# Optimization experiments

Hardware: AMD Instinct MI355X
Metric: run time of the kernel (lower is better)

Reference implementation:

```python
import jax, jax.numpy as jnp
import numpy as np

ALPHA = 0.2  # LeakyReLU negative slope used throughout
NEG = -9e15


def _leaky(x, a=ALPHA):
    return jnp.where(x >= 0, x, a * x)


def _gat_layer(h, adj, W, a, concat):
    # h: [N, Fin], W: [Fin, Fout], a: [2*Fout, 1]
    Wh = h @ W                                   # [N, Fout]
    d = W.shape[-1]
    e = _leaky(Wh @ a[:d] + (Wh @ a[d:]).T)      # [N, N]
    att = jax.nn.softmax(jnp.where(adj > 0, e, NEG), axis=1)
    out = att @ Wh                               # [N, Fout]
    return jax.nn.elu(out) if concat else out


def setup_inputs() -> dict:
    key = jax.random.key(0)
    ks = jax.random.split(key, 24)
    N, F, H, D1, O1 = 4096, 512, 4, 256, 64
    x = jax.random.normal(ks[0], (N, F), dtype=jnp.float32)
    adj = jax.random.bernoulli(ks[1], 0.02, (N, N))
    adj = (adj | adj.T | jnp.eye(N, dtype=bool)).astype(jnp.float32)
    observation = jax.random.randint(ks[2], (1, N), 0, 2, dtype=jnp.int32)
    s_mat = jax.random.uniform(ks[3], (N, N), dtype=jnp.float32)
    theta = jax.random.uniform(ks[4], (1, F), dtype=jnp.float32)
    g = lambda k, s, sc: (jax.random.normal(k, s, dtype=jnp.float32) * sc)
    return {
        'x': x, 'adj': adj, 'observation': observation, 's_mat': s_mat,
        'theta': theta,
        'Wh0': g(ks[5], (H, F, D1), 0.05), 'ah0': g(ks[6], (H, 2 * D1, 1), 0.05),
        'Wh1': g(ks[7], (H, D1, D1), 0.05), 'ah1': g(ks[8], (H, 2 * D1, 1), 0.05),
        'Wo0': g(ks[9], (H * D1, O1), 0.05), 'ao0': g(ks[10], (2 * O1, 1), 0.05),
        'Wo1': g(ks[11], (O1, 1), 0.2), 'ao1': g(ks[12], (2, 1), 0.2),
        'dW': g(ks[13], (2, 10), 0.5), 'dW0': g(ks[14], (1, 10), 0.5),
        'dW1': g(ks[15], (10, 20), 0.5), 'dW01': g(ks[16], (1, 20), 0.5),
        'dW2': g(ks[17], (20, 10), 0.5), 'dW02': g(ks[18], (1, 10), 0.5),
        'dV': g(ks[19], (10, 1), 0.5), 'dV0': g(ks[20], (1, 1), 0.5),
    }


def reference(x, adj, observation, s_mat, theta, Wh0, ah0, Wh1, ah1,
              Wo0, ao0, Wo1, ao1, dW, dW0, dW1, dW01, dW2, dW02, dV, dV0):
    # mergeState: add theta to rows in the seed set (observation[0] == 1)
    seed = (observation[0] == 1).astype(x.dtype)[:, None]  # [N,1]
    h_in = x + seed * theta

    # multi-head 2-layer attention stacks (concat=True -> elu inside)
    def head(W0, a0, W1, a1):
        h = _gat_layer(h_in, adj, W0, a0, True)
        return _gat_layer(h, adj, W1, a1, True)

    hh = jax.vmap(head)(Wh0, ah0, Wh1, ah1)                 # [H, N, D1]
    hcat = jnp.transpose(hh, (1, 0, 2)).reshape(h_in.shape[0], -1)  # [N, H*D1]

    # output attention stack (concat=False), then elu (GAT.forward)
    h = _gat_layer(hcat, adj, Wo0, ao0, False)
    h = _gat_layer(h, adj, Wo1, ao1, False)
    h_ = jax.nn.elu(h)                                      # [N, 1]

    # GAT_degree v2: degreeNN over [h_, degree]
    d_v = s_mat.sum(axis=1, keepdims=True)                  # [N, 1]
    x_ = jnp.concatenate([h_, d_v], axis=1)                 # [N, 2]
    h0 = _leaky(x_ @ dW + dW0)
    h1 = _leaky(h0 @ dW1 + dW01)
    h2 = _leaky(h1 @ dW2 + dW02)
    return _leaky(h2 @ dV + dV0)                            # [N, 1]
```

## Files before the change

### kernel.cpp

```cpp
#include <hip/hip_runtime.h>
#include <hip/hip_bf16.h>
#include <math.h>

#define MAXDEG 512

typedef short v8s __attribute__((ext_vector_type(8)));
typedef float v4f __attribute__((ext_vector_type(4)));
typedef float v2f __attribute__((ext_vector_type(2)));

__device__ __forceinline__ float blockReduceSum(float v) {
    __shared__ float sh[8];
    int lane = threadIdx.x & 63, w = threadIdx.x >> 6;
    for (int o = 32; o > 0; o >>= 1) v += __shfl_down(v, o);
    __syncthreads();
    if (lane == 0) sh[w] = v;
    __syncthreads();
    if (w == 0) {
        int nw = (blockDim.x + 63) >> 6;
        v = (lane < nw) ? sh[lane] : 0.f;
        for (int o = 4; o > 0; o >>= 1) v += __shfl_down(v, o);
        if (lane == 0) sh[0] = v;
    }
    __syncthreads();
    return sh[0];
}

__device__ __forceinline__ float blockReduceMax(float v) {
    __shared__ float sh[8];
    int lane = threadIdx.x & 63, w = threadIdx.x >> 6;
    for (int o = 32; o > 0; o >>= 1) v = fmaxf(v, __shfl_down(v, o));
    __syncthreads();
    if (lane == 0) sh[w] = v;
    __syncthreads();
    if (w == 0) {
        int nw = (blockDim.x + 63) >> 6;
        v = (lane < nw) ? sh[lane] : -3.4e38f;
        for (int o = 4; o > 0; o >>= 1) v = fmaxf(v, __shfl_down(v, o));
        if (lane == 0) sh[0] = v;
    }
    __syncthreads();
    return sh[0];
}

__device__ __forceinline__ v2f bf2f(unsigned int u) {
    union { unsigned int u; float f; } lo, hi;
    lo.u = u << 16;
    hi.u = u & 0xffff0000u;
    return (v2f){lo.f, hi.f};
}

__device__ __forceinline__ void acc_add(v2f* a, float p, const uint4& r) {
    v2f pp = (v2f){p, p};
    a[0] += pp * bf2f(r.x);
    a[1] += pp * bf2f(r.y);
    a[2] += pp * bf2f(r.z);
    a[3] += pp * bf2f(r.w);
}


__global__ void zero_f32(float* __restrict__ p, int n) {
    int i = blockIdx.x * 256 + threadIdx.x;
    if (i < n) p[i] = 0.f;
}

__global__ void csr_rowsum(const float* __restrict__ adj, const float* __restrict__ s,
                           int* __restrict__ colIdx, int* __restrict__ deg,
                           float* __restrict__ dv, int N) {
    int row = blockIdx.x;
    __shared__ int cnt;
    if (threadIdx.x == 0) cnt = 0;
    __syncthreads();
    const float* ar = adj + (size_t)row * N;
    const float* sr = s + (size_t)row * N;
    int* outp = colIdx + (size_t)row * MAXDEG;
    float psum = 0.f;
    for (int j = threadIdx.x; j < N; j += blockDim.x) {
        psum += sr[j];
        if (ar[j] > 0.f) {
            int p = atomicAdd(&cnt, 1);
            if (p < MAXDEG) outp[p] = j;
        }
    }
    psum = blockReduceSum(psum);
    __syncthreads();
    if (threadIdx.x == 0) {
        deg[row] = cnt < MAXDEG ? cnt : MAXDEG;
        dv[row] = psum;
    }
}

__global__ void hin_kernel(const float* __restrict__ x, const int* __restrict__ obs,
                           const float* __restrict__ theta, __hip_bfloat16* __restrict__ hin,
                           int NF) {
    int i = blockIdx.x * 256 + threadIdx.x;
    if (i >= NF) return;
    int n = i >> 9, f = i & 511;
    float v = x[i];
    if (obs[n] == 1) v += theta[f];
    hin[i] = __float2bfloat16(v);
}

__global__ void conv_wt(const float* __restrict__ W, __hip_bfloat16* __restrict__ Wt,
                        int K, int M) {
    int b = blockIdx.y;
    size_t i = (size_t)blockIdx.x * 256 + threadIdx.x;
    if (i >= (size_t)M * K) return;
    int mm = (int)(i / K), kk = (int)(i % K);
    Wt[(size_t)b * M * K + i] = __float2bfloat16(W[(size_t)b * K * M + (size_t)kk * M + mm]);
}

__global__ __launch_bounds__(256) void gemm_mfma(
    const __hip_bfloat16* __restrict__ A, const __hip_bfloat16* __restrict__ Bt,
    __hip_bfloat16* __restrict__ C, int N, int K, int M,
    size_t sA, size_t sB, size_t sC,
    const float* __restrict__ aVec, size_t aStride,
    float* __restrict__ el, float* __restrict__ er) {
    int b = blockIdx.z;
    const unsigned short* Ag = (const unsigned short*)(A + (size_t)b * sA);
    const unsigned short* Bg = (const unsigned short*)(Bt + (size_t)b * sB);
    __hip_bfloat16* Cg = C + (size_t)b * sC;
    const float* av = aVec + (size_t)b * aStride;

    __shared__ __align__(16) unsigned short As[64][40];
    __shared__ __align__(16) unsigned short Bs[64][40];

    const int tid = threadIdx.x;
    const int wave = tid >> 6, lane = tid & 63;
    const int row0 = blockIdx.y * 64, col0 = blockIdx.x * 64;
    const int sRow = tid >> 2;
    const int sOff = (tid & 3) * 8;
    const int m = lane & 15, quad = lane >> 4;

    v4f acc[4];
    #pragma unroll
    for (int c = 0; c < 4; c++) acc[c] = (v4f)(0.f);

    for (int k0 = 0; k0 < K; k0 += 32) {
        *(int4*)(&As[sRow][sOff]) =
            *(const int4*)(Ag + (size_t)(row0 + sRow) * K + k0 + sOff);
        *(int4*)(&Bs[sRow][sOff]) =
            *(const int4*)(Bg + (size_t)(col0 + sRow) * K + k0 + sOff);
        __syncthreads();
        v8s af = *(const v8s*)(&As[wave * 16 + m][quad * 8]);
        #pragma unroll
        for (int c = 0; c < 4; c++) {
            v8s bf = *(const v8s*)(&Bs[c * 16 + m][quad * 8]);
            acc[c] = __builtin_amdgcn_mfma_f32_16x16x32_bf16(af, bf, acc[c], 0, 0, 0);
        }
        __syncthreads();
    }
    #pragma unroll
    for (int c = 0; c < 4; c++)
        #pragma unroll
        for (int r = 0; r < 4; r++) {
            int row = row0 + wave * 16 + quad * 4 + r;
            int col = col0 + c * 16 + m;
            Cg[(size_t)row * M + col] = __float2bfloat16(acc[c][r]);
        }
    float ael[4], aer[4];
    #pragma unroll
    for (int c = 0; c < 4; c++) {
        ael[c] = av[col0 + c * 16 + m];
        aer[c] = av[M + col0 + c * 16 + m];
    }
    #pragma unroll
    for (int r = 0; r < 4; r++) {
        float pel = 0.f, per_ = 0.f;
        #pragma unroll
        for (int c = 0; c < 4; c++) {
            pel += acc[c][r] * ael[c];
            per_ += acc[c][r] * aer[c];
        }
        #pragma unroll
        for (int off = 1; off < 16; off <<= 1) {
            pel += __shfl_xor(pel, off);
            per_ += __shfl_xor(per_, off);
        }
        if (m == 0) {
            int row = row0 + wave * 16 + quad * 4 + r;
            atomicAdd(&el[(size_t)b * N + row], pel);
            atomicAdd(&er[(size_t)b * N + row], per_);
        }
    }
}

template<int D, int ACT, int HEADS>
__global__ __launch_bounds__(256) void attn_vec(
    const unsigned short* __restrict__ Wh, const float* __restrict__ el,
    const float* __restrict__ er, const int* __restrict__ colIdx,
    const int* __restrict__ deg, __hip_bfloat16* __restrict__ out,
    int N, size_t sWh, size_t sOut, int outRowStride) {
    constexpr int LPN = D / 8;
    constexpr int NPW = 64 / LPN;
    constexpr int STRIDE = 4 * NPW;

    int b, row;
    if (HEADS == 4) {
        int blk = blockIdx.x;
        b = (blk & 7) >> 1;
        row = ((blk >> 3) << 1) | (blk & 1);
    } else {
        b = 0;
        row = blockIdx.x;
    }
    const int tid = threadIdx.x;
    const unsigned short* whb = Wh + (size_t)b * sWh;
    const float* erb = er + (size_t)b * N;
    const float eln = el[(size_t)b * N + row];
    const int dc = deg[row];
    const int* ci = colIdx + (size_t)row * MAXDEG;

    __shared__ float2 spc[MAXDEG];
    __shared__ float redc[4 * D];

    float mx = -3.4e38f;
    for (int k = tid; k < dc; k += 256) {
        int j = ci[k];
        float s = eln + erb[j];
        s = fmaxf(s, 0.2f * s);
        spc[k] = make_float2(s, __int_as_float(j));
        mx = fmaxf(mx, s);
    }
    mx = blockReduceMax(mx);
    float l = 0.f;
    for (int k = tid; k < dc; k += 256) {
        float p = __expf(spc[k].x - mx);
        spc[k].x = p;
        l += p;
    }
    l = blockReduceSum(l);
    const float inv = 1.f / l;

    const int wave = tid >> 6, lane = tid & 63;
    const int sub = lane / LPN;
    const int dl = (lane % LPN) * 8;
    const unsigned short* wp = whb + dl;

    v2f a0[4], a1[4];
    #pragma unroll
    for (int i = 0; i < 4; i++) { a0[i] = (v2f)(0.f); a1[i] = (v2f)(0.f); }

    for (int k = wave * NPW + sub; k < dc; k += 2 * STRIDE) {
        float2 pc0 = spc[k];
        int j0 = __float_as_int(pc0.y);
        const uint4 r0 = *(const uint4*)(wp + (size_t)j0 * D);
        int k1 = k + STRIDE;
        float2 pc1 = (k1 < dc) ? spc[k1] : make_float2(0.f, pc0.y);
        int j1 = __float_as_int(pc1.y);
        const uint4 r1 = *(const uint4*)(wp + (size_t)j1 * D);
        acc_add(a0, pc0.x, r0);
        acc_add(a1, pc1.x, r1);
    }
    #pragma unroll
    for (int i = 0; i < 4; i++) a0[i] += a1[i];
    #pragma unroll
    for (int off = LPN; off < 64; off <<= 1)
        #pragma unroll
        for (int i = 0; i < 4; i++) {
            a0[i][0] += __shfl_xor(a0[i][0], off);
            a0[i][1] += __shfl_xor(a0[i][1], off);
        }
    __syncthreads();
    if (sub == 0)
        #pragma unroll
        for (int i = 0; i < 4; i++)
            *(float2*)(&redc[wave * D + dl + 2 * i]) = make_float2(a0[i][0], a0[i][1]);
    __syncthreads();
    if (tid < D) {
        float v = (redc[tid] + redc[D + tid] + redc[2 * D + tid] + redc[3 * D + tid]) * inv;
        if (ACT == 1) v = (v > 0.f) ? v : expm1f(v);
        out[(size_t)b * sOut + (size_t)row * outRowStride + tid] = __float2bfloat16(v);
    }
}

__global__ void attn_d1(const __hip_bfloat16* __restrict__ Wh, const float* __restrict__ el,
                        const float* __restrict__ er, const int* __restrict__ colIdx,
                        const int* __restrict__ deg, __hip_bfloat16* __restrict__ out, int N) {
    int row = blockIdx.x, tid = threadIdx.x;
    const float eln = el[row];
    const int dc = deg[row];
    const int* ci = colIdx + (size_t)row * MAXDEG;
    __shared__ float sp[MAXDEG];
    __shared__ int sc[MAXDEG];
    float mx = -3.4e38f;
    for (int k = tid; k < dc; k += blockDim.x) {
        int j = ci[k];
        sc[k] = j;
        float s = eln + er[j];
        s = fmaxf(s, 0.2f * s);
        sp[k] = s;
        mx = fmaxf(mx, s);
    }
    mx = blockReduceMax(mx);
    float l = 0.f, acc = 0.f;
    for (int k = tid; k < dc; k += blockDim.x) {
        float p = __expf(sp[k] - mx);
        l += p;
        acc += p * __bfloat162float(Wh[sc[k]]);
    }
    l = blockReduceSum(l);
    acc = blockReduceSum(acc);
    if (tid == 0) out[row] = __float2bfloat16(acc / l);
}

__global__ void matvec64_kernel(const __hip_bfloat16* __restrict__ h3,
                                const float* __restrict__ w,
                                const float* __restrict__ ao1,
                                __hip_bfloat16* __restrict__ out,
                                float* __restrict__ el4, float* __restrict__ er4, int N) {
    int row = blockIdx.x;
    float v = __bfloat162float(h3[(size_t)row * 64 + threadIdx.x]) * w[threadIdx.x];
    for (int o = 32; o > 0; o >>= 1) v += __shfl_down(v, o);
    if (threadIdx.x == 0) {
        out[row] = __float2bfloat16(v);
        el4[row] = v * ao1[0];
        er4[row] = v * ao1[1];
    }
}

__device__ __forceinline__ float leaky(float x) { return x >= 0.f ? x : 0.2f * x; }

__global__ void degree_nn(const __hip_bfloat16* __restrict__ h4, const float* __restrict__ dv,
                          const float* __restrict__ dW, const float* __restrict__ dW0,
                          const float* __restrict__ dW1, const float* __restrict__ dW01,
                          const float* __restrict__ dW2, const float* __restrict__ dW02,
                          const float* __restrict__ dV, const float* __restrict__ dV0,
                          float* __restrict__ out, int N) {
    int n = blockIdx.x * blockDim.x + threadIdx.x;
    if (n >= N) return;
    float h = __bfloat162float(h4[n]);
    h = (h > 0.f) ? h : expm1f(h);
    float d = dv[n];
    float t0[10], t1[20], t2[10];
    #pragma unroll
    for (int i = 0; i < 10; i++)
        t0[i] = leaky(h * dW[i] + d * dW[10 + i] + dW0[i]);
    #pragma unroll
    for (int j = 0; j < 20; j++) {
        float s = dW01[j];
        #pragma unroll
        for (int i = 0; i < 10; i++) s += t0[i] * dW1[i * 20 + j];
        t1[j] = leaky(s);
    }
    #pragma unroll
    for (int j = 0; j < 10; j++) {
        float s = dW02[j];
        #pragma unroll
        for (int i = 0; i < 20; i++) s += t1[i] * dW2[i * 10 + j];
        t2[j] = leaky(s);
    }
    float o = dV0[0];
    #pragma unroll
    for (int i = 0; i < 10; i++) o += t2[i] * dV[i];
    out[n] = leaky(o);
}

extern "C" void kernel_launch(void* const* d_in, const int* in_sizes, int n_in,
                              void* d_out, int out_size, void* d_ws, size_t ws_size,
                              hipStream_t stream) {
    const int N = 4096, F = 512, H = 4, D1 = 256, O1 = 64;
    const float* x     = (const float*)d_in[0];
    const float* adj   = (const float*)d_in[1];
    const int*   obs   = (const int*)  d_in[2];
    const float* s_mat = (const float*)d_in[3];
    const float* theta = (const float*)d_in[4];
    const float* Wh0   = (const float*)d_in[5];
    const float* ah0   = (const float*)d_in[6];
    const float* Wh1   = (const float*)d_in[7];
    const float* ah1   = (const float*)d_in[8];
    const float* Wo0   = (const float*)d_in[9];
    const float* ao0   = (const float*)d_in[10];
    const float* Wo1   = (const float*)d_in[11];
    const float* ao1   = (const float*)d_in[12];
    const float* dWp   = (const float*)d_in[13];
    const float* dW0p  = (const float*)d_in[14];
    const float* dW1p  = (const float*)d_in[15];
    const float* dW01p = (const float*)d_in[16];
    const float* dW2p  = (const float*)d_in[17];
    const float* dW02p = (const float*)d_in[18];
    const float* dVp   = (const float*)d_in[19];
    const float* dV0p  = (const float*)d_in[20];
    float* outp = (float*)d_out;

    char* ws = (char*)d_ws;
    auto alloc = [&](size_t bytes) {
        char* p = ws;
        ws += (bytes + 255) & ~(size_t)255;
        return p;
    };
    typedef __hip_bfloat16 bf;
    bf* hin   = (bf*)alloc((size_t)N * F * 2);
    bf* whA   = (bf*)alloc((size_t)H * N * D1 * 2);
    bf* hb    = (bf*)alloc((size_t)H * N * D1 * 2);
    bf* hcat  = (bf*)alloc((size_t)N * H * D1 * 2);
    bf* o1Wh  = (bf*)alloc((size_t)N * O1 * 2);
    bf* o1o   = (bf*)alloc((size_t)N * O1 * 2);
    bf* o2Wh  = (bf*)alloc((size_t)N * 2);
    bf* o2o   = (bf*)alloc((size_t)N * 2);
    bf* Wh0t  = (bf*)alloc((size_t)H * F * D1 * 2);
    bf* Wh1t  = (bf*)alloc((size_t)H * D1 * D1 * 2);
    bf* Wo0t  = (bf*)alloc((size_t)H * D1 * O1 * 2);
    int elerN = 4 * H * N + 2 * N;
    float* elerZ = (float*)alloc((size_t)elerN * 4);
    float* el1 = elerZ;
    float* er1 = el1 + H * N;
    float* el2 = er1 + H * N;
    float* er2 = el2 + H * N;
    float* el3 = er2 + H * N;
    float* er3 = el3 + N;
    float* el4 = (float*)alloc((size_t)N * 4);
    float* er4 = (float*)alloc((size_t)N * 4);
    float* dv  = (float*)alloc((size_t)N * 4);
    int* colIdx = (int*)alloc((size_t)N * MAXDEG * 4);
    int* deg    = (int*)alloc((size_t)N * 4);

    zero_f32<<<(elerN + 255) / 256, 256, 0, stream>>>(elerZ, elerN);
    csr_rowsum<<<N, 256, 0, stream>>>(adj, s_mat, colIdx, deg, dv, N);
    hin_kernel<<<(N * F + 255) / 256, 256, 0, stream>>>(x, obs, theta, hin, N * F);
    conv_wt<<<dim3((F * D1 + 255) / 256, H), 256, 0, stream>>>(Wh0, Wh0t, F, D1);
    conv_wt<<<dim3((D1 * D1 + 255) / 256, H), 256, 0, stream>>>(Wh1, Wh1t, D1, D1);
    conv_wt<<<dim3((H * D1 * O1 + 255) / 256, 1), 256, 0, stream>>>(Wo0, Wo0t, H * D1, O1);

    gemm_mfma<<<dim3(D1 / 64, N / 64, H), 256, 0, stream>>>(
        hin, Wh0t, whA, N, F, D1, 0, (size_t)D1 * F, (size_t)N * D1,
        ah0, (size_t)2 * D1, el1, er1);
    attn_vec<256, 1, 4><<<N * H, 256, 0, stream>>>(
        (const unsigned short*)whA, el1, er1, colIdx, deg, hb,
        N, (size_t)N * D1, (size_t)N * D1, D1);

    gemm_mfma<<<dim3(D1 / 64, N / 64, H), 256, 0, stream>>>(
        hb, Wh1t, whA, N, D1, D1, (size_t)N * D1, (size_t)D1 * D1, (size_t)N * D1,
        ah1, (size_t)2 * D1, el2, er2);
    attn_vec<256, 1, 4><<<N * H, 256, 0, stream>>>(
        (const unsigned short*)whA, el2, er2, colIdx, deg, hcat,
        N, (size_t)N * D1, (size_t)D1, H * D1);

    gemm_mfma<<<dim3(O1 / 64, N / 64, 1), 256, 0, stream>>>(
        hcat, Wo0t, o1Wh, N, H * D1, O1, 0, 0, 0,
        ao0, 0, el3, er3);
    attn_vec<64, 0, 1><<<N, 256, 0, stream>>>(
        (const unsigned short*)o1Wh, el3, er3, colIdx, deg, o1o, N, 0, 0, O1);

    matvec64_kernel<<<N, 64, 0, stream>>>(o1o, Wo1, ao1, o2Wh, el4, er4, N);
    attn_d1<<<N, 256, 0, stream>>>(o2Wh, el4, er4, colIdx, deg, o2o, N);

    degree_nn<<<(N + 255) / 256, 256, 0, stream>>>(o2o, dv, dWp, dW0p, dW1p,
        dW01p, dW2p, dW02p, dVp, dV0p, outp, N);
}
```

Measured before the change: 443.6 us.

## Use 128x128 MFMA GEMM tiles, fuse prep kernels, pad attention gather loop

The first two per-head GEMMs now use a new 128x128 tile kernel in which each wave computes a 64x64 sub-tile, giving more MFMA work per shared-memory load. The input merge and three weight-transpose kernels are fused into one prep launch. In the attention gather, the neighbor list is padded to a multiple of the unroll stride and stores precomputed row offsets, which removes the bounds check and a multiply from the inner loop. The larger tiles cut the GEMM grid to far fewer blocks, which may hurt occupancy, and the prep kernel now hardcodes the problem dimensions.

```diff
diff --git a/kernel.cpp b/kernel.cpp
--- a/kernel.cpp
+++ b/kernel.cpp
@@ -7,6 +7,7 @@
 typedef short v8s __attribute__((ext_vector_type(8)));
 typedef float v4f __attribute__((ext_vector_type(4)));
 typedef float v2f __attribute__((ext_vector_type(2)));
+typedef __hip_bfloat16 bf;
 
 __device__ __forceinline__ float blockReduceSum(float v) {
     __shared__ float sh[8];
@@ -89,36 +90,142 @@
     }
 }
 
-__global__ void hin_kernel(const float* __restrict__ x, const int* __restrict__ obs,
-                           const float* __restrict__ theta, __hip_bfloat16* __restrict__ hin,
-                           int NF) {
+__global__ void prep(const float* __restrict__ x, const int* __restrict__ obs,
+                     const float* __restrict__ theta,
+                     const float* __restrict__ Wh0, const float* __restrict__ Wh1,
+                     const float* __restrict__ Wo0,
+                     bf* __restrict__ hin, bf* __restrict__ Wh0t,
+                     bf* __restrict__ Wh1t, bf* __restrict__ Wo0t) {
+    const int n0 = 4096 * 512;
+    const int n1 = 4 * 512 * 256;
+    const int n2 = 4 * 256 * 256;
+    const int n3 = 1024 * 64;
     int i = blockIdx.x * 256 + threadIdx.x;
-    if (i >= NF) return;
-    int n = i >> 9, f = i & 511;
-    float v = x[i];
-    if (obs[n] == 1) v += theta[f];
-    hin[i] = __float2bfloat16(v);
-}
-
-__global__ void conv_wt(const float* __restrict__ W, __hip_bfloat16* __restrict__ Wt,
-                        int K, int M) {
-    int b = blockIdx.y;
-    size_t i = (size_t)blockIdx.x * 256 + threadIdx.x;
-    if (i >= (size_t)M * K) return;
-    int mm = (int)(i / K), kk = (int)(i % K);
-    Wt[(size_t)b * M * K + i] = __float2bfloat16(W[(size_t)b * K * M + (size_t)kk * M + mm]);
-}
-
-__global__ __launch_bounds__(256) void gemm_mfma(
-    const __hip_bfloat16* __restrict__ A, const __hip_bfloat16* __restrict__ Bt,
-    __hip_bfloat16* __restrict__ C, int N, int K, int M,
+    if (i < n0) {
+        int n = i >> 9, f = i & 511;
+        float v = x[i];
+        if (obs[n] == 1) v += theta[f];
+        hin[i] = __float2bfloat16(v);
+    } else if (i < n0 + n1) {
+        int t = i - n0;
+        int b = t / (512 * 256), r = t % (512 * 256);
+        int mm = r >> 9, kk = r & 511;
+        Wh0t[t] = __float2bfloat16(Wh0[b * 512 * 256 + kk * 256 + mm]);
+    } else if (i < n0 + n1 + n2) {
+        int t = i - n0 - n1;
+        int b = t >> 16, r = t & 65535;
+        int mm = r >> 8, kk = r & 255;
+        Wh1t[t] = __float2bfloat16(Wh1[b * 65536 + kk * 256 + mm]);
+    } else if (i < n0 + n1 + n2 + n3) {
+        int t = i - n0 - n1 - n2;
+        int mm = t >> 10, kk = t & 1023;
+        Wo0t[t] = __float2bfloat16(Wo0[kk * 64 + mm]);
+    }
+}
+
+__global__ __launch_bounds__(256) void gemm_mfma128(
+    const bf* __restrict__ A, const bf* __restrict__ Bt,
+    bf* __restrict__ C, int N, int K, int M,
     size_t sA, size_t sB, size_t sC,
     const float* __restrict__ aVec, size_t aStride,
     float* __restrict__ el, float* __restrict__ er) {
     int b = blockIdx.z;
     const unsigned short* Ag = (const unsigned short*)(A + (size_t)b * sA);
     const unsigned short* Bg = (const unsigned short*)(Bt + (size_t)b * sB);
-    __hip_bfloat16* Cg = C + (size_t)b * sC;
+    bf* Cg = C + (size_t)b * sC;
+    const float* av = aVec + (size_t)b * aStride;
+
+    __shared__ __align__(16) unsigned short As[128][40];
+    __shared__ __align__(16) unsigned short Bs[128][40];
+
+    const int tid = threadIdx.x;
+    const int wave = tid >> 6, lane = tid & 63;
+    const int wm = wave >> 1, wn = wave & 1;
+    const int row0 = blockIdx.y * 128, col0 = blockIdx.x * 128;
+    const int lr = tid >> 2;
+    const int lo = (tid & 3) * 8;
+    const int m = lane & 15, quad = lane >> 4;
+
+    v4f acc[4][4];
+    #pragma unroll
+    for (int i = 0; i < 4; i++)
+        #pragma unroll
+        for (int c = 0; c < 4; c++) acc[i][c] = (v4f)(0.f);
+
+    for (int k0 = 0; k0 < K; k0 += 32) {
+        *(int4*)(&As[lr][lo]) =
+            *(const int4*)(Ag + (size_t)(row0 + lr) * K + k0 + lo);
+        *(int4*)(&As[lr + 64][lo]) =
+            *(const int4*)(Ag + (size_t)(row0 + 64 + lr) * K + k0 + lo);
+        *(int4*)(&Bs[lr][lo]) =
+            *(const int4*)(Bg + (size_t)(col0 + lr) * K + k0 + lo);
+        *(int4*)(&Bs[lr + 64][lo]) =
+            *(const int4*)(Bg + (size_t)(col0 + 64 + lr) * K + k0 + lo);
+        __syncthreads();
+        v8s af[4], bfv[4];
+        #pragma unroll
+        for (int i = 0; i < 4; i++)
+            af[i] = *(const v8s*)(&As[wm * 64 + i * 16 + m][quad * 8]);
+        #pragma unroll
+        for (int c = 0; c < 4; c++)
+            bfv[c] = *(const v8s*)(&Bs[wn * 64 + c * 16 + m][quad * 8]);
+        #pragma unroll
+        for (int i = 0; i < 4; i++)
+            #pragma unroll
+            for (int c = 0; c < 4; c++)
+                acc[i][c] = __builtin_amdgcn_mfma_f32_16x16x32_bf16(
+                    af[i], bfv[c], acc[i][c], 0, 0, 0);
+        __syncthreads();
+    }
+    #pragma unroll
+    for (int i = 0; i < 4; i++)
+        #pragma unroll
+        for (int c = 0; c < 4; c++)
+            #pragma unroll
+            for (int r = 0; r < 4; r++) {
+                int row = row0 + wm * 64 + i * 16 + quad * 4 + r;
+                int col = col0 + wn * 64 + c * 16 + m;
+                Cg[(size_t)row * M + col] = __float2bfloat16(acc[i][c][r]);
+            }
+    float ael[4], aer[4];
+    #pragma unroll
+    for (int c = 0; c < 4; c++) {
+        ael[c] = av[col0 + wn * 64 + c * 16 + m];
+        aer[c] = av[M + col0 + wn * 64 + c * 16 + m];
+    }
+    #pragma unroll
+    for (int i = 0; i < 4; i++)
+        #pragma unroll
+        for (int r = 0; r < 4; r++) {
+            float pel = 0.f, per_ = 0.f;
+            #pragma unroll
+            for (int c = 0; c < 4; c++) {
+                pel += acc[i][c][r] * ael[c];
+                per_ += acc[i][c][r] * aer[c];
+            }
+            #pragma unroll
+            for (int off = 1; off < 16; off <<= 1) {
+                pel += __shfl_xor(pel, off);
+                per_ += __shfl_xor(per_, off);
+            }
+            if (m == 0) {
+                int row = row0 + wm * 64 + i * 16 + quad * 4 + r;
+                atomicAdd(&el[(size_t)b * N + row], pel);
+                atomicAdd(&er[(size_t)b * N + row], per_);
+            }
+        }
+}
+
+__global__ __launch_bounds__(256) void gemm_mfma64(
+    const bf* __restrict__ A, const bf* __restrict__ Bt,
+    bf* __restrict__ C, int N, int K, int M,
+    size_t sA, size_t sB, size_t sC,
+    const float* __restrict__ aVec, size_t aStride,
+    float* __restrict__ el, float* __restrict__ er) {
+    int b = blockIdx.z;
+    const unsigned short* Ag = (const unsigned short*)(A + (size_t)b * sA);
+    const unsigned short* Bg = (const unsigned short*)(Bt + (size_t)b * sB);
+    bf* Cg = C + (size_t)b * sC;
     const float* av = aVec + (size_t)b * aStride;
 
     __shared__ __align__(16) unsigned short As[64][40];
@@ -144,8 +251,8 @@
         v8s af = *(const v8s*)(&As[wave * 16 + m][quad * 8]);
         #pragma unroll
         for (int c = 0; c < 4; c++) {
-            v8s bf = *(const v8s*)(&Bs[c * 16 + m][quad * 8]);
-            acc[c] = __builtin_amdgcn_mfma_f32_16x16x32_bf16(af, bf, acc[c], 0, 0, 0);
+            v8s bfv = *(const v8s*)(&Bs[c * 16 + m][quad * 8]);
+            acc[c] = __builtin_amdgcn_mfma_f32_16x16x32_bf16(af, bfv, acc[c], 0, 0, 0);
         }
         __syncthreads();
     }
@@ -188,11 +295,12 @@
 __global__ __launch_bounds__(256) void attn_vec(
     const unsigned short* __restrict__ Wh, const float* __restrict__ el,
     const float* __restrict__ er, const int* __restrict__ colIdx,
-    const int* __restrict__ deg, __hip_bfloat16* __restrict__ out,
+    const int* __restrict__ deg, bf* __restrict__ out,
     int N, size_t sWh, size_t sOut, int outRowStride) {
     constexpr int LPN = D / 8;
     constexpr int NPW = 64 / LPN;
     constexpr int STRIDE = 4 * NPW;
+    constexpr int PAD = 2 * STRIDE;
 
     int b, row;
     if (HEADS == 4) {
@@ -208,19 +316,22 @@
     const float* erb = er + (size_t)b * N;
     const float eln = el[(size_t)b * N + row];
     const int dc = deg[row];
+    const int dcp = (dc + PAD - 1) & ~(PAD - 1);
     const int* ci = colIdx + (size_t)row * MAXDEG;
 
-    __shared__ float2 spc[MAXDEG];
-    __shared__ float redc[4 * D];
+    __shared__ __align__(16) float2 spc[MAXDEG];
+    __shared__ __align__(16) float redc[4 * D];
 
     float mx = -3.4e38f;
     for (int k = tid; k < dc; k += 256) {
         int j = ci[k];
         float s = eln + erb[j];
         s = fmaxf(s, 0.2f * s);
-        spc[k] = make_float2(s, __int_as_float(j));
+        spc[k] = make_float2(s, __int_as_float(j * D));
         mx = fmaxf(mx, s);
     }
+    for (int k = dc + tid; k < dcp; k += 256)
+        spc[k] = make_float2(0.f, __int_as_float(0));
     mx = blockReduceMax(mx);
     float l = 0.f;
     for (int k = tid; k < dc; k += 256) {
@@ -240,14 +351,11 @@
     #pragma unroll
     for (int i = 0; i < 4; i++) { a0[i] = (v2f)(0.f); a1[i] = (v2f)(0.f); }
 
-    for (int k = wave * NPW + sub; k < dc; k += 2 * STRIDE) {
+    for (int k = wave * NPW + sub; k < dcp; k += 2 * STRIDE) {
         float2 pc0 = spc[k];
-        int j0 = __float_as_int(pc0.y);
-        const uint4 r0 = *(const uint4*)(wp + (size_t)j0 * D);
-        int k1 = k + STRIDE;
-        float2 pc1 = (k1 < dc) ? spc[k1] : make_float2(0.f, pc0.y);
-        int j1 = __float_as_int(pc1.y);
-        const uint4 r1 = *(const uint4*)(wp + (size_t)j1 * D);
+        float2 pc1 = spc[k + STRIDE];
+        const uint4 r0 = *(const uint4*)(wp + __float_as_int(pc0.y));
+        const uint4 r1 = *(const uint4*)(wp + __float_as_int(pc1.y));
         acc_add(a0, pc0.x, r0);
         acc_add(a1, pc1.x, r1);
     }
@@ -273,9 +381,9 @@
     }
 }
 
-__global__ void attn_d1(const __hip_bfloat16* __restrict__ Wh, const float* __restrict__ el,
+__global__ void attn_d1(const bf* __restrict__ Wh, const float* __restrict__ el,
                         const float* __restrict__ er, const int* __restrict__ colIdx,
-                        const int* __restrict__ deg, __hip_bfloat16* __restrict__ out, int N) {
+                        const int* __restrict__ deg, bf* __restrict__ out, int N) {
     int row = blockIdx.x, tid = threadIdx.x;
     const float eln = el[row];
     const int dc = deg[row];
@@ -303,10 +411,10 @@
     if (tid == 0) out[row] = __float2bfloat16(acc / l);
 }
 
-__global__ void matvec64_kernel(const __hip_bfloat16* __restrict__ h3,
+__global__ void matvec64_kernel(const bf* __restrict__ h3,
                                 const float* __restrict__ w,
                                 const float* __restrict__ ao1,
-                                __hip_bfloat16* __restrict__ out,
+                                bf* __restrict__ out,
                                 float* __restrict__ el4, float* __restrict__ er4, int N) {
     int row = blockIdx.x;
     float v = __bfloat162float(h3[(size_t)row * 64 + threadIdx.x]) * w[threadIdx.x];
@@ -320,7 +428,7 @@
 
 __device__ __forceinline__ float leaky(float x) { return x >= 0.f ? x : 0.2f * x; }
 
-__global__ void degree_nn(const __hip_bfloat16* __restrict__ h4, const float* __restrict__ dv,
+__global__ void degree_nn(const bf* __restrict__ h4, const float* __restrict__ dv,
                           const float* __restrict__ dW, const float* __restrict__ dW0,
                           const float* __restrict__ dW1, const float* __restrict__ dW01,
                           const float* __restrict__ dW2, const float* __restrict__ dW02,
@@ -388,18 +496,17 @@
         ws += (bytes + 255) & ~(size_t)255;
         return p;
     };
-    typedef __hip_bfloat16 bf;
-    bf* hin   = (bf*)alloc((size_t)N * F * 2);
-    bf* whA   = (bf*)alloc((size_t)H * N * D1 * 2);
-    bf* hb    = (bf*)alloc((size_t)H * N * D1 * 2);
-    bf* hcat  = (bf*)alloc((size_t)N * H * D1 * 2);
-    bf* o1Wh  = (bf*)alloc((size_t)N * O1 * 2);
-    bf* o1o   = (bf*)alloc((size_t)N * O1 * 2);
-    bf* o2Wh  = (bf*)alloc((size_t)N * 2);
-    bf* o2o   = (bf*)alloc((size_t)N * 2);
-    bf* Wh0t  = (bf*)alloc((size_t)H * F * D1 * 2);
-    bf* Wh1t  = (bf*)alloc((size_t)H * D1 * D1 * 2);
-    bf* Wo0t  = (bf*)alloc((size_t)H * D1 * O1 * 2);
+    bf* hin     = (bf*)alloc((size_t)N * F * 2);
+    bf* whA     = (bf*)alloc((size_t)H * N * D1 * 2);
+    bf* hb      = (bf*)alloc((size_t)H * N * D1 * 2);
+    bf* hcat    = (bf*)alloc((size_t)N * H * D1 * 2);
+    bf* o1Wh    = (bf*)alloc((size_t)N * O1 * 2);
+    bf* o1o     = (bf*)alloc((size_t)N * O1 * 2);
+    bf* o2Wh    = (bf*)alloc((size_t)N * 2);
+    bf* o2o     = (bf*)alloc((size_t)N * 2);
+    bf* Wh0t    = (bf*)alloc((size_t)H * F * D1 * 2);
+    bf* Wh1t    = (bf*)alloc((size_t)H * D1 * D1 * 2);
+    bf* Wo0t    = (bf*)alloc((size_t)H * D1 * O1 * 2);
     int elerN = 4 * H * N + 2 * N;
     float* elerZ = (float*)alloc((size_t)elerN * 4);
     float* el1 = elerZ;
@@ -416,26 +523,27 @@
 
     zero_f32<<<(elerN + 255) / 256, 256, 0, stream>>>(elerZ, elerN);
     csr_rowsum<<<N, 256, 0, stream>>>(adj, s_mat, colIdx, deg, dv, N);
-    hin_kernel<<<(N * F + 255) / 256, 256, 0, stream>>>(x, obs, theta, hin, N * F);
-    conv_wt<<<dim3((F * D1 + 255) / 256, H), 256, 0, stream>>>(Wh0, Wh0t, F, D1);
-    conv_wt<<<dim3((D1 * D1 + 255) / 256, H), 256, 0, stream>>>(Wh1, Wh1t, D1, D1);
-    conv_wt<<<dim3((H * D1 * O1 + 255) / 256, 1), 256, 0, stream>>>(Wo0, Wo0t, H * D1, O1);
-
-    gemm_mfma<<<dim3(D1 / 64, N / 64, H), 256, 0, stream>>>(
+    {
+        const int totalPrep = N * F + H * F * D1 + H * D1 * D1 + H * D1 * O1;
+        prep<<<(totalPrep + 255) / 256, 256, 0, stream>>>(
+            x, obs, theta, Wh0, Wh1, Wo0, hin, Wh0t, Wh1t, Wo0t);
+    }
+
+    gemm_mfma128<<<dim3(D1 / 128, N / 128, H), 256, 0, stream>>>(
         hin, Wh0t, whA, N, F, D1, 0, (size_t)D1 * F, (size_t)N * D1,
         ah0, (size_t)2 * D1, el1, er1);
     attn_vec<256, 1, 4><<<N * H, 256, 0, stream>>>(
         (const unsigned short*)whA, el1, er1, colIdx, deg, hb,
         N, (size_t)N * D1, (size_t)N * D1, D1);
 
-    gemm_mfma<<<dim3(D1 / 64, N / 64, H), 256, 0, stream>>>(
+    gemm_mfma128<<<dim3(D1 / 128, N / 128, H), 256, 0, stream>>>(
         hb, Wh1t, whA, N, D1, D1, (size_t)N * D1, (size_t)D1 * D1, (size_t)N * D1,
         ah1, (size_t)2 * D1, el2, er2);
     attn_vec<256, 1, 4><<<N * H, 256, 0, stream>>>(
         (const unsigned short*)whA, el2, er2, colIdx, deg, hcat,
         N, (size_t)N * D1, (size_t)D1, H * D1);
 
-    gemm_mfma<<<dim3(O1 / 64, N / 64, 1), 256, 0, stream>>>(
+    gemm_mfma64<<<dim3(O1 / 64, N / 64, 1), 256, 0, stream>>>(
         hcat, Wo0t, o1Wh, N, H * D1, O1, 0, 0, 0,
         ao0, 0, el3, er3);
     attn_vec<64, 0, 1><<<N, 256, 0, stream>>>(
```

After: 427.8 us. -3.5%, faster.
